# Performance work log

Measured on AMD Instinct MI355X. Metric: run time of the kernel, lower is better.

Reference implementation:

```python
import jax, jax.numpy as jnp
import numpy as np

INPUT_SIZE = 768
HIDDEN = [512, 256, 128]
LATENT = 32
NUM_LEVELS = 3
CODEBOOK_SIZE = 256
BATCH = 131072


def _init_linear(key, d_in, d_out):
    kw, kb = jax.random.split(key)
    lim = 1.0 / np.sqrt(d_in)
    W = jax.random.uniform(kw, (d_in, d_out), jnp.float32, -lim, lim)
    b = jax.random.uniform(kb, (d_out,), jnp.float32, -lim, lim)
    return W, b


def setup_inputs() -> dict:
    key = jax.random.key(0)
    keys = jax.random.split(key, 16)
    inp = {"x": jax.random.normal(keys[0], (BATCH, INPUT_SIZE), jnp.float32)}
    enc_dims = [INPUT_SIZE] + HIDDEN + [LATENT]          # 768->512->256->128->32
    dec_dims = [LATENT] + HIDDEN[::-1] + [INPUT_SIZE]     # 32->128->256->512->768
    for i in range(4):
        W, b = _init_linear(keys[1 + i], enc_dims[i], enc_dims[i + 1])
        inp[f"enc_W{i}"], inp[f"enc_b{i}"] = W, b
        W, b = _init_linear(keys[6 + i], dec_dims[i], dec_dims[i + 1])
        inp[f"dec_W{i}"], inp[f"dec_b{i}"] = W, b
    inp["codebooks"] = jax.random.normal(keys[12], (NUM_LEVELS, CODEBOOK_SIZE, LATENT), jnp.float32)
    return inp


def _mlp(x, Ws, bs):
    # Linear -> ReLU (-> Dropout p=0, identity) between layers, final layer linear.
    n = len(Ws)
    for i in range(n):
        x = x @ Ws[i] + bs[i]
        if i < n - 1:
            x = jax.nn.relu(x)
    return x


def _quantize(z, codebooks):
    # Residual vector quantization over NUM_LEVELS codebooks.
    L, K, D = codebooks.shape
    r = z
    idxs, rs, es = [], [], []
    for l in range(L):
        c = codebooks[l]                                  # [K, D]
        # squared-distance argmin (same argmin as cdist)
        d = jnp.sum(r * r, axis=-1, keepdims=True) - 2.0 * (r @ c.T) + jnp.sum(c * c, axis=-1)
        idx = jnp.argmin(d, axis=-1)                      # [B]
        e = c[idx]                                        # [B, D] gather
        idxs.append(idx)
        rs.append(r)
        es.append(e)
        r = r - e
    quantized = jnp.stack(idxs, axis=1)                   # [B, L] int codes
    r_stack = jnp.stack(rs, axis=1)                       # [B, L, D] residual inputs per level
    e_stack = jnp.stack(es, axis=1)                       # [B, L, D] selected embeddings
    sum_e = jnp.sum(e_stack, axis=1)                      # [B, D]
    # straight-through estimator
    z_hat = z + jax.lax.stop_gradient(sum_e - z)
    counts = jnp.sum(jax.nn.one_hot(quantized, K, dtype=jnp.float32), axis=0)  # [L, K] usage
    return quantized, r_stack, e_stack, z_hat, counts


def reference(x,
              enc_W0, enc_b0, enc_W1, enc_b1, enc_W2, enc_b2, enc_W3, enc_b3,
              dec_W0, dec_b0, dec_W1, dec_b1, dec_W2, dec_b2, dec_W3, dec_b3,
              codebooks):
    encoded = _mlp(x, [enc_W0, enc_W1, enc_W2, enc_W3], [enc_b0, enc_b1, enc_b2, enc_b3])
    quantized, r, e, z_hat, counts = _quantize(encoded, codebooks)
    decoded = _mlp(z_hat, [dec_W0, dec_W1, dec_W2, dec_W3], [dec_b0, dec_b1, dec_b2, dec_b3])
    return decoded, r, e, counts, quantized
```

## Files before the change

### kernel.cpp

```cpp
#include <hip/hip_runtime.h>
#include <hip/hip_bf16.h>
#include <cfloat>

#define B_TOTAL 131072
#define IN_DIM  768
#define NLEV    3
#define KCODE   256

typedef unsigned short u16;
typedef unsigned int   u32;
typedef __attribute__((ext_vector_type(8))) short bf16x8;
typedef __attribute__((ext_vector_type(4))) float f32x4;

#define GLOAD_LDS(g, l)                                                        \
    __builtin_amdgcn_global_load_lds(                                          \
        (const __attribute__((address_space(1))) u32*)(g),                     \
        (__attribute__((address_space(3))) u32*)(l), 16, 0, 0)

__device__ __forceinline__ u16 f2bf(float x) {
    union { __hip_bfloat16 h; u16 u; } c;
    c.h = __float2bfloat16(x);
    return c.u;
}
__device__ __forceinline__ float bf2f(u32 lo16) {
    union { u32 v; float f; } c;
    c.v = lo16 << 16;
    return c.f;
}
__device__ __forceinline__ u32 pack2(float a, float b) {
    return (u32)f2bf(a) | ((u32)f2bf(b) << 16);
}

template<int K, int N, bool AF32, bool RELU, bool OUTF32>
__global__ __launch_bounds__(256)
void gemm_mfma(const void* __restrict__ A_, const u16* __restrict__ Wt,
               const float* __restrict__ bias, void* __restrict__ C_)
{
    constexpr int NK  = K / 32;
    constexpr int NCB = N / 128;
    __shared__ u16 As[3][4096];
    __shared__ u16 Bs[3][4096];

    const int tid  = threadIdx.x;
    const int lane = tid & 63;
    const int wid  = tid >> 6;
    const int wrow = wid >> 1, wcol = wid & 1;

    const u32 nwg  = gridDim.x;
    const u32 orig = blockIdx.x;
    const u32 xcd = orig & 7u, q8 = nwg >> 3, r8 = nwg & 7u;
    const u32 wg = (xcd < r8 ? xcd * (q8 + 1) : r8 * (q8 + 1) + (xcd - r8) * q8)
                 + (orig >> 3);
    const int col0 = (int)(wg % NCB) * 128;
    const int row0 = (int)(wg / NCB) * 128;

    const u16*   Ab = (const u16*)A_;
    const float* Af = (const float*)A_;

    f32x4 acc[4][4];
    #pragma unroll
    for (int i = 0; i < 4; ++i)
        #pragma unroll
        for (int j = 0; j < 4; ++j) acc[i][j] = (f32x4){0.f, 0.f, 0.f, 0.f};

    auto stage_one = [&](u16* dstbase, const u16* src) {
        #pragma unroll
        for (int i = 0; i < 2; ++i) {
            const u32 o   = (u32)(i * 4096 + wid * 1024 + lane * 16);
            const u32 row = o >> 6;
            const u32 cbs = (o & 63u) ^ ((row & 3u) << 4);
            GLOAD_LDS((const char*)(src + (size_t)row * K) + cbs,
                      dstbase + (i * 2048 + wid * 512));
        }
    };
    auto stage_tile = [&](int buf, int kt) {
        stage_one(&Bs[buf][0], Wt + (size_t)col0 * K + kt * 32);
        stage_one(&As[buf][0], Ab + (size_t)row0 * K + kt * 32);
    };

    auto compute = [&](int buf) {
        const char* Ab8 = (const char*)&As[buf][0];
        const char* Bb8 = (const char*)&Bs[buf][0];
        const int kb = (lane >> 4) * 16;
        bf16x8 af[4], bf[4];
        #pragma unroll
        for (int mf = 0; mf < 4; ++mf) {
            const int r = wrow * 64 + mf * 16 + (lane & 15);
            af[mf] = *(const bf16x8*)(Ab8 + r * 64 + (kb ^ ((r & 3) << 4)));
        }
        #pragma unroll
        for (int nf = 0; nf < 4; ++nf) {
            const int r = wcol * 64 + nf * 16 + (lane & 15);
            bf[nf] = *(const bf16x8*)(Bb8 + r * 64 + (kb ^ ((r & 3) << 4)));
        }
        #pragma unroll
        for (int mf = 0; mf < 4; ++mf)
            #pragma unroll
            for (int nf = 0; nf < 4; ++nf)
                acc[mf][nf] = __builtin_amdgcn_mfma_f32_16x16x32_bf16(
                    af[mf], bf[nf], acc[mf][nf], 0, 0, 0);
    };

    if constexpr (AF32) {
        float4 fa[4];
        auto loadA = [&](int kt) {
            const int row = tid >> 1;
            const int ce0 = (tid & 1) * 16;
            const float* s = &Af[(size_t)(row0 + row) * K + kt * 32 + ce0];
            fa[0] = *(const float4*)(s + 0);
            fa[1] = *(const float4*)(s + 4);
            fa[2] = *(const float4*)(s + 8);
            fa[3] = *(const float4*)(s + 12);
        };
        auto writeA = [&](int buf) {
            const int row = tid >> 1;
            const int cb0 = (tid & 1) * 32;
            const int sw  = (row & 3) << 4;
            char* lb = (char*)&As[buf][0] + row * 64;
            *(uint4*)(lb + ((cb0 + 0) ^ sw)) = make_uint4(
                pack2(fa[0].x, fa[0].y), pack2(fa[0].z, fa[0].w),
                pack2(fa[1].x, fa[1].y), pack2(fa[1].z, fa[1].w));
            *(uint4*)(lb + ((cb0 + 16) ^ sw)) = make_uint4(
                pack2(fa[2].x, fa[2].y), pack2(fa[2].z, fa[2].w),
                pack2(fa[3].x, fa[3].y), pack2(fa[3].z, fa[3].w));
        };

        loadA(0);
        stage_one(&Bs[0][0], Wt + (size_t)col0 * K);
        writeA(0);
        if (NK > 1) {
            loadA(1);
            stage_one(&Bs[1][0], Wt + (size_t)col0 * K + 32);
        }

        #pragma unroll 1
        for (int kt = 0; kt < NK; ++kt) {
            if (kt == NK - 1) asm volatile("s_waitcnt vmcnt(0) lgkmcnt(0)");
            else              asm volatile("s_waitcnt vmcnt(6) lgkmcnt(0)");
            __builtin_amdgcn_sched_barrier(0);
            __builtin_amdgcn_s_barrier();
            __builtin_amdgcn_sched_barrier(0);
            if (kt + 1 < NK) writeA((kt + 1) % 3);
            if (kt + 2 < NK) {
                loadA(kt + 2);
                stage_one(&Bs[(kt + 2) % 3][0],
                          Wt + (size_t)col0 * K + (kt + 2) * 32);
            }
            compute(kt % 3);
        }
    } else {
        stage_tile(0, 0);
        if (NK > 1) stage_tile(1, 1);
        int cb_ = 0, sb_ = 2;
        #pragma unroll 1
        for (int kt = 0; kt < NK; ++kt) {
            if (kt == NK - 1) asm volatile("s_waitcnt vmcnt(0)");
            else              asm volatile("s_waitcnt vmcnt(4)");
            __builtin_amdgcn_sched_barrier(0);
            __builtin_amdgcn_s_barrier();
            __builtin_amdgcn_sched_barrier(0);
            if (kt + 2 < NK) stage_tile(sb_, kt + 2);
            compute(cb_);
            cb_ = (cb_ == 2) ? 0 : cb_ + 1;
            sb_ = (sb_ == 2) ? 0 : sb_ + 1;
        }
    }

    #pragma unroll
    for (int nf = 0; nf < 4; ++nf) {
        const int col = col0 + wcol * 64 + nf * 16 + (lane & 15);
        const float bv = bias[col];
        #pragma unroll
        for (int mf = 0; mf < 4; ++mf) {
            const int rbase = row0 + wrow * 64 + mf * 16 + (lane >> 4) * 4;
            #pragma unroll
            for (int r = 0; r < 4; ++r) {
                float o = acc[mf][nf][r] + bv;
                if (RELU) o = fmaxf(o, 0.f);
                if constexpr (OUTF32)
                    ((float*)C_)[(size_t)(rbase + r) * N + col] = o;
                else
                    ((u16*)C_)[(size_t)(rbase + r) * N + col] = f2bf(o);
            }
        }
    }
}

template<int K, int N>
__global__ __launch_bounds__(256)
void wcvt(const float* __restrict__ W, u16* __restrict__ Wt)
{
    const int idx = blockIdx.x * 256 + threadIdx.x;
    const int k = idx / N, n = idx - k * N;
    Wt[(size_t)n * K + k] = f2bf(W[idx]);
}

__global__ __launch_bounds__(256)
void vq_kernel(const u16* __restrict__ h3, const float* __restrict__ eW3,
               const float* __restrict__ eb3, const float* __restrict__ cb,
               float* __restrict__ r_out, float* __restrict__ e_out,
               float* __restrict__ q_out, u16* __restrict__ se_ws,
               u32* __restrict__ ghist, size_t grow_base)
{
    __shared__ float W3[128 * 32];
    __shared__ float ebv[32];
    __shared__ float clds[256 * 36];
    __shared__ float cc2[256];
    __shared__ u32   lh[NLEV * KCODE];

    const int tid = threadIdx.x;
    const size_t lrow = (size_t)blockIdx.x * 256 + tid;
    const size_t grow = grow_base + lrow;

    for (int i = tid; i < 128 * 32; i += 256) W3[i] = eW3[i];
    if (tid < 32) ebv[tid] = eb3[tid];
    for (int i = tid; i < NLEV * KCODE; i += 256) lh[i] = 0;
    __syncthreads();

    float r[32];
    #pragma unroll
    for (int j = 0; j < 32; ++j) r[j] = ebv[j];
    {
        const u32* hrow = (const u32*)h3 + lrow * 64;
        #pragma unroll 2
        for (int k2 = 0; k2 < 64; ++k2) {
            const u32 v = hrow[k2];
            const float x0 = bf2f(v & 0xffffu), x1 = bf2f(v >> 16);
            const float* w0 = &W3[(2 * k2) * 32];
            const float* w1 = &W3[(2 * k2 + 1) * 32];
            #pragma unroll
            for (int j4 = 0; j4 < 8; ++j4) {
                const float4 a = *(const float4*)&w0[4 * j4];
                const float4 b = *(const float4*)&w1[4 * j4];
                r[4*j4+0] = fmaf(x1, b.x, fmaf(x0, a.x, r[4*j4+0]));
                r[4*j4+1] = fmaf(x1, b.y, fmaf(x0, a.y, r[4*j4+1]));
                r[4*j4+2] = fmaf(x1, b.z, fmaf(x0, a.z, r[4*j4+2]));
                r[4*j4+3] = fmaf(x1, b.w, fmaf(x0, a.w, r[4*j4+3]));
            }
        }
    }

    float z0[32];
    #pragma unroll
    for (int j = 0; j < 32; ++j) z0[j] = r[j];

    #pragma unroll 1
    for (int l = 0; l < NLEV; ++l) {
        __syncthreads();
        {
            const float* cl = cb + ((size_t)l * KCODE + tid) * 32;
            float s = 0.f;
            #pragma unroll
            for (int m = 0; m < 8; ++m) {
                const float4 v = *(const float4*)&cl[4 * m];
                *(float4*)&clds[tid * 36 + 4 * m] = v;
                s = fmaf(v.x, v.x, s); s = fmaf(v.y, v.y, s);
                s = fmaf(v.z, v.z, s); s = fmaf(v.w, v.w, s);
            }
            cc2[tid] = -0.5f * s;
        }
        __syncthreads();

        float best = -FLT_MAX;
        int   bidx = 0;
        #pragma unroll 1
        for (int k = 0; k < KCODE; ++k) {
            const float* ck = &clds[k * 36];
            float d0 = 0.f, d1 = 0.f, d2 = 0.f, d3 = 0.f;
            #pragma unroll
            for (int m = 0; m < 8; m += 4) {
                const float4 v0 = *(const float4*)&ck[4 * (m + 0)];
                const float4 v1 = *(const float4*)&ck[4 * (m + 1)];
                const float4 v2 = *(const float4*)&ck[4 * (m + 2)];
                const float4 v3 = *(const float4*)&ck[4 * (m + 3)];
                d0 = fmaf(r[4*m+0],  v0.x, d0); d0 = fmaf(r[4*m+1],  v0.y, d0);
                d0 = fmaf(r[4*m+2],  v0.z, d0); d0 = fmaf(r[4*m+3],  v0.w, d0);
                d1 = fmaf(r[4*m+4],  v1.x, d1); d1 = fmaf(r[4*m+5],  v1.y, d1);
                d1 = fmaf(r[4*m+6],  v1.z, d1); d1 = fmaf(r[4*m+7],  v1.w, d1);
                d2 = fmaf(r[4*m+8],  v2.x, d2); d2 = fmaf(r[4*m+9],  v2.y, d2);
                d2 = fmaf(r[4*m+10], v2.z, d2); d2 = fmaf(r[4*m+11], v2.w, d2);
                d3 = fmaf(r[4*m+12], v3.x, d3); d3 = fmaf(r[4*m+13], v3.y, d3);
                d3 = fmaf(r[4*m+14], v3.z, d3); d3 = fmaf(r[4*m+15], v3.w, d3);
            }
            const float s = ((d0 + d1) + (d2 + d3)) + cc2[k];
            if (s > best) { best = s; bidx = k; }
        }

        const size_t base = (grow * NLEV + l) * 32;
        const float* ce = &clds[bidx * 36];
        #pragma unroll
        for (int m = 0; m < 8; ++m) {
            const float4 ev = *(const float4*)&ce[4 * m];
            *(float4*)&r_out[base + 4 * m] =
                make_float4(r[4*m+0], r[4*m+1], r[4*m+2], r[4*m+3]);
            *(float4*)&e_out[base + 4 * m] = ev;
            r[4*m+0] -= ev.x; r[4*m+1] -= ev.y;
            r[4*m+2] -= ev.z; r[4*m+3] -= ev.w;
        }
        q_out[grow * NLEV + l] = (float)bidx;
        atomicAdd(&lh[l * KCODE + bidx], 1u);
    }

    u32* sed = (u32*)se_ws + lrow * 16;
    #pragma unroll
    for (int m = 0; m < 16; ++m)
        sed[m] = pack2(z0[2*m] - r[2*m], z0[2*m+1] - r[2*m+1]);

    __syncthreads();
    for (int i = tid; i < NLEV * KCODE; i += 256)
        if (lh[i]) atomicAdd(&ghist[i], lh[i]);
}

__global__ void zero_hist(u32* h) {
    if (threadIdx.x < NLEV * KCODE) h[threadIdx.x] = 0;
}
__global__ void counts_fin(const u32* __restrict__ g, float* __restrict__ o) {
    if (threadIdx.x < NLEV * KCODE) o[threadIdx.x] = (float)g[threadIdx.x];
}

__global__ __launch_bounds__(256)
void counts_k(const float* __restrict__ q, float* __restrict__ cnt)
{
    const int l = blockIdx.x >> 8;
    const int k = blockIdx.x & 255;
    const float pat = (float)k;
    int c = 0;
    for (int i = threadIdx.x; i < B_TOTAL; i += 256)
        c += (q[(size_t)i * NLEV + l] == pat) ? 1 : 0;
    __shared__ int red[256];
    red[threadIdx.x] = c;
    __syncthreads();
    for (int s = 128; s > 0; s >>= 1) {
        if (threadIdx.x < s) red[threadIdx.x] += red[threadIdx.x + s];
        __syncthreads();
    }
    if (threadIdx.x == 0)
        cnt[blockIdx.x] = (float)red[0];
}

template<int K, int N, bool RELU, bool AGLOBAL>
static __device__ __forceinline__
void layer16(const float* __restrict__ A, size_t grow0,
             const float* __restrict__ W, const float* __restrict__ bias,
             float* __restrict__ C)
{
    constexpr int QPT = N / 128;
    const int tr = threadIdx.x >> 5;
    const int tc = threadIdx.x & 31;
    float acc[2][QPT * 4];
    #pragma unroll
    for (int i = 0; i < 2; ++i)
        #pragma unroll
        for (int j = 0; j < QPT * 4; ++j) acc[i][j] = 0.f;
    #pragma unroll 2
    for (int k0 = 0; k0 < K; k0 += 4) {
        float4 av[2];
        #pragma unroll
        for (int i = 0; i < 2; ++i) {
            if (AGLOBAL)
                av[i] = *(const float4*)&A[(grow0 + tr * 2 + i) * (size_t)K + k0];
            else
                av[i] = *(const float4*)&A[(tr * 2 + i) * K + k0];
        }
        #pragma unroll
        for (int kk = 0; kk < 4; ++kk) {
            #pragma unroll
            for (int q = 0; q < QPT; ++q) {
                const float4 w4 = *(const float4*)&W[(size_t)(k0 + kk) * N + 4 * (tc + 32 * q)];
                #pragma unroll
                for (int i = 0; i < 2; ++i) {
                    const float a = ((const float*)&av[i])[kk];
                    acc[i][4*q+0] = fmaf(a, w4.x, acc[i][4*q+0]);
                    acc[i][4*q+1] = fmaf(a, w4.y, acc[i][4*q+1]);
                    acc[i][4*q+2] = fmaf(a, w4.z, acc[i][4*q+2]);
                    acc[i][4*q+3] = fmaf(a, w4.w, acc[i][4*q+3]);
                }
            }
        }
    }
    #pragma unroll
    for (int q = 0; q < QPT; ++q) {
        const float4 b4 = *(const float4*)&bias[4 * (tc + 32 * q)];
        #pragma unroll
        for (int i = 0; i < 2; ++i) {
            float4 o;
            o.x = acc[i][4*q+0] + b4.x; o.y = acc[i][4*q+1] + b4.y;
            o.z = acc[i][4*q+2] + b4.z; o.w = acc[i][4*q+3] + b4.w;
            if (RELU) {
                o.x = fmaxf(o.x, 0.f); o.y = fmaxf(o.y, 0.f);
                o.z = fmaxf(o.z, 0.f); o.w = fmaxf(o.w, 0.f);
            }
            *(float4*)&C[(tr * 2 + i) * N + 4 * (tc + 32 * q)] = o;
        }
    }
}

static __device__ __forceinline__
void layer_final16(const float* __restrict__ A, const float* __restrict__ W,
                   const float* __restrict__ bias, float* __restrict__ Cg, size_t grow0)
{
    constexpr int QPT = 6;
    const int tr = threadIdx.x >> 5;
    const int tc = threadIdx.x & 31;
    float acc[2][QPT * 4];
    #pragma unroll
    for (int i = 0; i < 2; ++i)
        #pragma unroll
        for (int j = 0; j < QPT * 4; ++j) acc[i][j] = 0.f;
    #pragma unroll 2
    for (int k0 = 0; k0 < 512; k0 += 4) {
        float4 av[2];
        #pragma unroll
        for (int i = 0; i < 2; ++i)
            av[i] = *(const float4*)&A[(tr * 2 + i) * 512 + k0];
        #pragma unroll
        for (int kk = 0; kk < 4; ++kk) {
            #pragma unroll
            for (int q = 0; q < QPT; ++q) {
                const float4 w4 = *(const float4*)&W[(size_t)(k0 + kk) * 768 + 4 * (tc + 32 * q)];
                #pragma unroll
                for (int i = 0; i < 2; ++i) {
                    const float a = ((const float*)&av[i])[kk];
                    acc[i][4*q+0] = fmaf(a, w4.x, acc[i][4*q+0]);
                    acc[i][4*q+1] = fmaf(a, w4.y, acc[i][4*q+1]);
                    acc[i][4*q+2] = fmaf(a, w4.z, acc[i][4*q+2]);
                    acc[i][4*q+3] = fmaf(a, w4.w, acc[i][4*q+3]);
                }
            }
        }
    }
    #pragma unroll
    for (int q = 0; q < QPT; ++q) {
        const float4 b4 = *(const float4*)&bias[4 * (tc + 32 * q)];
        #pragma unroll
        for (int i = 0; i < 2; ++i) {
            float4 s;
            s.x = acc[i][4*q+0] + b4.x; s.y = acc[i][4*q+1] + b4.y;
            s.z = acc[i][4*q+2] + b4.z; s.w = acc[i][4*q+3] + b4.w;
            *(float4*)&Cg[(grow0 + tr * 2 + i) * (size_t)768 + 4 * (tc + 32 * q)] = s;
        }
    }
}

static __device__ __forceinline__
void layer_narrow16(const float* __restrict__ A, const float* __restrict__ W,
                    const float* __restrict__ bias, float* __restrict__ Z)
{
    const int row = threadIdx.x >> 4;
    const int g   = threadIdx.x & 15;
    float a0 = 0.f, a1 = 0.f;
    #pragma unroll 4
    for (int k0 = 0; k0 < 128; k0 += 4) {
        const float4 av = *(const float4*)&A[row * 128 + k0];
        #pragma unroll
        for (int kk = 0; kk < 4; ++kk) {
            const float2 w2 = *(const float2*)&W[(k0 + kk) * 32 + 2 * g];
            const float a = ((const float*)&av)[kk];
            a0 = fmaf(a, w2.x, a0);
            a1 = fmaf(a, w2.y, a1);
        }
    }
    Z[row * 36 + 2 * g + 0] = a0 + bias[2 * g + 0];
    Z[row * 36 + 2 * g + 1] = a1 + bias[2 * g + 1];
}

__global__ __launch_bounds__(256)
void enc_vq_kernel(const float* __restrict__ x,
                   const float* __restrict__ eW0, const float* __restrict__ eb0,
                   const float* __restrict__ eW1, const float* __restrict__ eb1,
                   const float* __restrict__ eW2, const float* __restrict__ eb2,
                   const float* __restrict__ eW3, const float* __restrict__ eb3,
                   const float* __restrict__ cb,
                   float* __restrict__ r_out, float* __restrict__ e_out,
                   float* __restrict__ q_out)
{
    __shared__ __align__(16) char smem[59648];
    float* h1   = (float*)(smem);
    float* h2   = (float*)(smem + 32768);
    float* h3   = (float*)(smem + 49152);
    float* z    = (float*)(smem + 57344);
    float* clds = (float*)(smem);
    float* cc   = (float*)(smem + 36864);

    const size_t grow0 = (size_t)blockIdx.x * 16;
    layer16<768, 512, true, true >(x,  grow0, eW0, eb0, h1);
    __syncthreads();
    layer16<512, 256, true, false>(h1, 0,     eW1, eb1, h2);
    __syncthreads();
    layer16<256, 128, true, false>(h2, 0,     eW2, eb2, h3);
    __syncthreads();
    layer_narrow16(h3, eW3, eb3, z);

    const int row = threadIdx.x >> 4;
    const int g   = threadIdx.x & 15;
    const size_t grow = grow0 + row;

    #pragma unroll 1
    for (int l = 0; l < NLEV; ++l) {
        __syncthreads();
        {
            const float* cl = cb + (size_t)l * KCODE * 32;
            const int t = threadIdx.x;
            float s = 0.f;
            #pragma unroll
            for (int m = 0; m < 8; ++m) {
                const float4 v = *(const float4*)&cl[t * 32 + 4 * m];
                *(float4*)&clds[t * 36 + 4 * m] = v;
                s = fmaf(v.x, v.x, s); s = fmaf(v.y, v.y, s);
                s = fmaf(v.z, v.z, s); s = fmaf(v.w, v.w, s);
            }
            cc[t] = s;
        }
        __syncthreads();

        float r[32];
        #pragma unroll
        for (int m = 0; m < 8; ++m) {
            const float4 v = *(const float4*)&z[row * 36 + 4 * m];
            r[4*m+0] = v.x; r[4*m+1] = v.y; r[4*m+2] = v.z; r[4*m+3] = v.w;
        }
        float rr = 0.f;
        #pragma unroll
        for (int j = 0; j < 32; ++j) rr = fmaf(r[j], r[j], rr);

        float best = FLT_MAX;
        int   bidx = 0x7fffffff;
        #pragma unroll 1
        for (int t = 0; t < 16; ++t) {
            const int k = g + 16 * t;
            const float* ck = &clds[k * 36];
            float d0 = 0.f, d1 = 0.f, d2 = 0.f, d3 = 0.f;
            #pragma unroll
            for (int m = 0; m < 8; m += 4) {
                const float4 v0 = *(const float4*)&ck[4 * (m + 0)];
                const float4 v1 = *(const float4*)&ck[4 * (m + 1)];
                const float4 v2 = *(const float4*)&ck[4 * (m + 2)];
                const float4 v3 = *(const float4*)&ck[4 * (m + 3)];
                d0 = fmaf(r[4*m+0],  v0.x, d0); d0 = fmaf(r[4*m+1],  v0.y, d0);
                d0 = fmaf(r[4*m+2],  v0.z, d0); d0 = fmaf(r[4*m+3],  v0.w, d0);
                d1 = fmaf(r[4*m+4],  v1.x, d1); d1 = fmaf(r[4*m+5],  v1.y, d1);
                d1 = fmaf(r[4*m+6],  v1.z, d1); d1 = fmaf(r[4*m+7],  v1.w, d1);
                d2 = fmaf(r[4*m+8],  v2.x, d2); d2 = fmaf(r[4*m+9],  v2.y, d2);
                d2 = fmaf(r[4*m+10], v2.z, d2); d2 = fmaf(r[4*m+11], v2.w, d2);
                d3 = fmaf(r[4*m+12], v3.x, d3); d3 = fmaf(r[4*m+13], v3.y, d3);
                d3 = fmaf(r[4*m+14], v3.z, d3); d3 = fmaf(r[4*m+15], v3.w, d3);
            }
            const float dot = (d0 + d1) + (d2 + d3);
            const float d = (rr - 2.f * dot) + cc[k];
            if (d < best || (d == best && k < bidx)) { best = d; bidx = k; }
        }
        #pragma unroll
        for (int off = 1; off < 16; off <<= 1) {
            const float ob = __shfl_xor(best, off);
            const int   oi = __shfl_xor(bidx, off);
            if (ob < best || (ob == best && oi < bidx)) { best = ob; bidx = oi; }
        }

        const float evx = clds[bidx * 36 + 2 * g + 0];
        const float evy = clds[bidx * 36 + 2 * g + 1];
        *(float2*)&r_out[(grow * NLEV + l) * 32 + 2 * g] = make_float2(r[2*g], r[2*g+1]);
        *(float2*)&e_out[(grow * NLEV + l) * 32 + 2 * g] = make_float2(evx, evy);
        if (g == 0) q_out[grow * NLEV + l] = (float)bidx;
        z[row * 36 + 2 * g + 0] = r[2 * g + 0] - evx;
        z[row * 36 + 2 * g + 1] = r[2 * g + 1] - evy;
    }
}

__global__ __launch_bounds__(256)
void dec_kernel(const float* __restrict__ e_in,
                const float* __restrict__ dW0, const float* __restrict__ db0,
                const float* __restrict__ dW1, const float* __restrict__ db1,
                const float* __restrict__ dW2, const float* __restrict__ db2,
                const float* __restrict__ dW3, const float* __restrict__ db3,
                float* __restrict__ dec_out)
{
    __shared__ __align__(16) char smem[59392];
    float* h3 = (float*)(smem);
    float* h2 = (float*)(smem + 32768);
    float* h1 = (float*)(smem + 49152);
    float* se = (float*)(smem + 57344);

    const size_t grow0 = (size_t)blockIdx.x * 16;
    const int row = threadIdx.x >> 4;
    const int g   = threadIdx.x & 15;
    {
        const size_t base = ((grow0 + row) * NLEV) * 32 + 2 * g;
        float s0 = 0.f, s1 = 0.f;
        #pragma unroll
        for (int l = 0; l < NLEV; ++l) {
            const float2 v = *(const float2*)&e_in[base + l * 32];
            s0 += v.x; s1 += v.y;
        }
        se[row * 32 + 2 * g + 0] = s0;
        se[row * 32 + 2 * g + 1] = s1;
    }
    __syncthreads();
    layer16<32,  128, true, false>(se, 0, dW0, db0, h1);
    __syncthreads();
    layer16<128, 256, true, false>(h1, 0, dW1, db1, h2);
    __syncthreads();
    layer16<256, 512, true, false>(h2, 0, dW2, db2, h3);
    __syncthreads();
    layer_final16(h3, dW3, db3, dec_out, grow0);
}

extern "C" void kernel_launch(void* const* d_in, const int* in_sizes, int n_in,
                              void* d_out, int out_size, void* d_ws, size_t ws_size,
                              hipStream_t stream)
{
    (void)in_sizes; (void)n_in; (void)out_size;
    const float* x  = (const float*)d_in[0];
    const float* cb = (const float*)d_in[17];
    const float *eW[4], *eb[4], *dW[4], *db[4];
    for (int i = 0; i < 4; ++i) {
        eW[i] = (const float*)d_in[1 + 4 * i];
        eb[i] = (const float*)d_in[2 + 4 * i];
        dW[i] = (const float*)d_in[3 + 4 * i];
        db[i] = (const float*)d_in[4 + 4 * i];
    }

    float* out = (float*)d_out;
    const size_t OFF_R = (size_t)B_TOTAL * IN_DIM;
    const size_t OFF_E = OFF_R + (size_t)B_TOTAL * NLEV * 32;
    const size_t OFF_C = OFF_E + (size_t)B_TOTAL * NLEV * 32;
    const size_t OFF_Q = OFF_C + (size_t)NLEV * KCODE;

    const size_t WTB = 2236416;
    size_t R = 0;
    for (size_t cand = 131072; cand >= 2048; cand >>= 1)
        if (WTB + cand * 3648 + 4096 <= ws_size) { R = cand; break; }

    if (R && d_ws) {
        u16* Wp   = (u16*)d_ws;
        u16* WtE0 = Wp;
        u16* WtE1 = WtE0 + 393216;
        u16* WtE2 = WtE1 + 131072;
        u16* WtD0 = WtE2 + 32768;
        u16* WtD1 = WtD0 + 4096;
        u16* WtD2 = WtD1 + 32768;
        u16* WtD3 = WtD2 + 131072;
        u16* h1   = WtD3 + 393216;
        u16* h2   = h1 + R * 512;
        u16* h3   = h2 + R * 256;
        u16* se   = h3 + R * 128;
        u16* d1   = se + R * 32;
        u16* d2   = d1 + R * 128;
        u16* d3   = d2 + R * 256;
        u32* ghist = (u32*)(d3 + R * 512);

        wcvt<768, 512><<<dim3((768 * 512) / 256), 256, 0, stream>>>(eW[0], WtE0);
        wcvt<512, 256><<<dim3((512 * 256) / 256), 256, 0, stream>>>(eW[1], WtE1);
        wcvt<256, 128><<<dim3((256 * 128) / 256), 256, 0, stream>>>(eW[2], WtE2);
        wcvt<32,  128><<<dim3((32 * 128) / 256),  256, 0, stream>>>(dW[0], WtD0);
        wcvt<128, 256><<<dim3((128 * 256) / 256), 256, 0, stream>>>(dW[1], WtD1);
        wcvt<256, 512><<<dim3((256 * 512) / 256), 256, 0, stream>>>(dW[2], WtD2);
        wcvt<512, 768><<<dim3((512 * 768) / 256), 256, 0, stream>>>(dW[3], WtD3);
        zero_hist<<<1, 768, 0, stream>>>(ghist);

        const int nch = B_TOTAL / (int)R;
        const int MB = (int)R / 128;
        for (int c = 0; c < nch; ++c) {
            const size_t rb = (size_t)c * R;
            gemm_mfma<768, 512, true,  true,  false><<<dim3(4 * MB), 256, 0, stream>>>(
                x + rb * 768, WtE0, eb[0], h1);
            gemm_mfma<512, 256, false, true,  false><<<dim3(2 * MB), 256, 0, stream>>>(
                h1, WtE1, eb[1], h2);
            gemm_mfma<256, 128, false, true,  false><<<dim3(1 * MB), 256, 0, stream>>>(
                h2, WtE2, eb[2], h3);
            vq_kernel<<<dim3((int)R / 256), 256, 0, stream>>>(
                h3, eW[3], eb[3], cb,
                out + OFF_R, out + OFF_E, out + OFF_Q, se, ghist, rb);
            gemm_mfma<32,  128, false, true,  false><<<dim3(1 * MB), 256, 0, stream>>>(
                se, WtD0, db[0], d1);
            gemm_mfma<128, 256, false, true,  false><<<dim3(2 * MB), 256, 0, stream>>>(
                d1, WtD1, db[1], d2);
            gemm_mfma<256, 512, false, true,  false><<<dim3(4 * MB), 256, 0, stream>>>(
                d2, WtD2, db[2], d3);
            gemm_mfma<512, 768, false, false, true ><<<dim3(6 * MB), 256, 0, stream>>>(
                d3, WtD3, db[3], out + rb * 768);
        }
        counts_fin<<<1, 768, 0, stream>>>(ghist, out + OFF_C);
    } else {
        enc_vq_kernel<<<dim3(B_TOTAL / 16), 256, 0, stream>>>(
            x, eW[0], eb[0], eW[1], eb[1], eW[2], eb[2], eW[3], eb[3], cb,
            out + OFF_R, out + OFF_E, out + OFF_Q);
        counts_k<<<dim3(NLEV * KCODE), 256, 0, stream>>>(out + OFF_Q, out + OFF_C);
        dec_kernel<<<dim3(B_TOTAL / 16), 256, 0, stream>>>(
            out + OFF_E, dW[0], db[0], dW[1], db[1], dW[2], db[2], dW[3], db[3], out);
    }
}
```

Baseline: 862.6 us.

## Enlarge GEMM block tile to 256x128 with 8 waves and MFMA priority

The MFMA GEMM block grows from 128x128 to 256x128 output rows by moving to 512 threads (8 waves), each wave still computing a 64x64 sub-tile. One staged weight (B) tile is now shared by twice as many rows, which halves B global/LDS staging per output and halves the number of workgroups launched. The A staging and vmcnt wait counts are adjusted to the new load counts, and s_setprio is raised around the MFMA loop to favour matrix issue. LDS per block rises to about 72KB and the grid shrinks, which may cut occupancy and leave CUs idle on the smaller layers.

```diff
diff --git a/kernel.cpp b/kernel.cpp
--- a/kernel.cpp
+++ b/kernel.cpp
@@ -32,19 +32,20 @@
 }
 
 template<int K, int N, bool AF32, bool RELU, bool OUTF32>
-__global__ __launch_bounds__(256)
+__global__ __launch_bounds__(512)
 void gemm_mfma(const void* __restrict__ A_, const u16* __restrict__ Wt,
                const float* __restrict__ bias, void* __restrict__ C_)
 {
     constexpr int NK  = K / 32;
     constexpr int NCB = N / 128;
-    __shared__ u16 As[3][4096];
+    __shared__ u16 As[3][8192];
     __shared__ u16 Bs[3][4096];
 
     const int tid  = threadIdx.x;
     const int lane = tid & 63;
     const int wid  = tid >> 6;
-    const int wrow = wid >> 1, wcol = wid & 1;
+    const int wrow = wid >> 1;
+    const int wcol = wid & 1;
 
     const u32 nwg  = gridDim.x;
     const u32 orig = blockIdx.x;
@@ -52,7 +53,7 @@
     const u32 wg = (xcd < r8 ? xcd * (q8 + 1) : r8 * (q8 + 1) + (xcd - r8) * q8)
                  + (orig >> 3);
     const int col0 = (int)(wg % NCB) * 128;
-    const int row0 = (int)(wg / NCB) * 128;
+    const int row0 = (int)(wg / NCB) * 256;
 
     const u16*   Ab = (const u16*)A_;
     const float* Af = (const float*)A_;
@@ -63,19 +64,26 @@
         #pragma unroll
         for (int j = 0; j < 4; ++j) acc[i][j] = (f32x4){0.f, 0.f, 0.f, 0.f};
 
-    auto stage_one = [&](u16* dstbase, const u16* src) {
+    auto stage_B = [&](u16* dstbase, const u16* src) {
+        const u32 o   = (u32)(tid * 16);
+        const u32 row = o >> 6;
+        const u32 cbs = (o & 63u) ^ ((row & 3u) << 4);
+        GLOAD_LDS((const char*)(src + (size_t)row * K) + cbs,
+                  dstbase + wid * 512);
+    };
+    auto stage_A = [&](u16* dstbase, const u16* src) {
         #pragma unroll
         for (int i = 0; i < 2; ++i) {
-            const u32 o   = (u32)(i * 4096 + wid * 1024 + lane * 16);
+            const u32 o   = (u32)(i * 8192 + tid * 16);
             const u32 row = o >> 6;
             const u32 cbs = (o & 63u) ^ ((row & 3u) << 4);
             GLOAD_LDS((const char*)(src + (size_t)row * K) + cbs,
-                      dstbase + (i * 2048 + wid * 512));
+                      dstbase + (i * 4096 + wid * 512));
         }
     };
     auto stage_tile = [&](int buf, int kt) {
-        stage_one(&Bs[buf][0], Wt + (size_t)col0 * K + kt * 32);
-        stage_one(&As[buf][0], Ab + (size_t)row0 * K + kt * 32);
+        stage_B(&Bs[buf][0], Wt + (size_t)col0 * K + kt * 32);
+        stage_A(&As[buf][0], Ab + (size_t)row0 * K + kt * 32);
     };
 
     auto compute = [&](int buf) {
@@ -93,12 +101,14 @@
             const int r = wcol * 64 + nf * 16 + (lane & 15);
             bf[nf] = *(const bf16x8*)(Bb8 + r * 64 + (kb ^ ((r & 3) << 4)));
         }
+        __builtin_amdgcn_s_setprio(1);
         #pragma unroll
         for (int mf = 0; mf < 4; ++mf)
             #pragma unroll
             for (int nf = 0; nf < 4; ++nf)
                 acc[mf][nf] = __builtin_amdgcn_mfma_f32_16x16x32_bf16(
                     af[mf], bf[nf], acc[mf][nf], 0, 0, 0);
+        __builtin_amdgcn_s_setprio(0);
     };
 
     if constexpr (AF32) {
@@ -126,25 +136,25 @@
         };
 
         loadA(0);
-        stage_one(&Bs[0][0], Wt + (size_t)col0 * K);
+        stage_B(&Bs[0][0], Wt + (size_t)col0 * K);
         writeA(0);
         if (NK > 1) {
             loadA(1);
-            stage_one(&Bs[1][0], Wt + (size_t)col0 * K + 32);
+            stage_B(&Bs[1][0], Wt + (size_t)col0 * K + 32);
         }
 
         #pragma unroll 1
         for (int kt = 0; kt < NK; ++kt) {
             if (kt == NK - 1) asm volatile("s_waitcnt vmcnt(0) lgkmcnt(0)");
-            else              asm volatile("s_waitcnt vmcnt(6) lgkmcnt(0)");
+            else              asm volatile("s_waitcnt vmcnt(5) lgkmcnt(0)");
             __builtin_amdgcn_sched_barrier(0);
             __builtin_amdgcn_s_barrier();
             __builtin_amdgcn_sched_barrier(0);
             if (kt + 1 < NK) writeA((kt + 1) % 3);
             if (kt + 2 < NK) {
                 loadA(kt + 2);
-                stage_one(&Bs[(kt + 2) % 3][0],
-                          Wt + (size_t)col0 * K + (kt + 2) * 32);
+                stage_B(&Bs[(kt + 2) % 3][0],
+                        Wt + (size_t)col0 * K + (kt + 2) * 32);
             }
             compute(kt % 3);
         }
@@ -155,7 +165,7 @@
         #pragma unroll 1
         for (int kt = 0; kt < NK; ++kt) {
             if (kt == NK - 1) asm volatile("s_waitcnt vmcnt(0)");
-            else              asm volatile("s_waitcnt vmcnt(4)");
+            else              asm volatile("s_waitcnt vmcnt(3)");
             __builtin_amdgcn_sched_barrier(0);
             __builtin_amdgcn_s_barrier();
             __builtin_amdgcn_sched_barrier(0);
@@ -658,25 +668,25 @@
         zero_hist<<<1, 768, 0, stream>>>(ghist);
 
         const int nch = B_TOTAL / (int)R;
-        const int MB = (int)R / 128;
+        const int MB2 = (int)R / 256;
         for (int c = 0; c < nch; ++c) {
             const size_t rb = (size_t)c * R;
-            gemm_mfma<768, 512, true,  true,  false><<<dim3(4 * MB), 256, 0, stream>>>(
+            gemm_mfma<768, 512, true,  true,  false><<<dim3(4 * MB2), 512, 0, stream>>>(
                 x + rb * 768, WtE0, eb[0], h1);
-            gemm_mfma<512, 256, false, true,  false><<<dim3(2 * MB), 256, 0, stream>>>(
+            gemm_mfma<512, 256, false, true,  false><<<dim3(2 * MB2), 512, 0, stream>>>(
                 h1, WtE1, eb[1], h2);
-            gemm_mfma<256, 128, false, true,  false><<<dim3(1 * MB), 256, 0, stream>>>(
+            gemm_mfma<256, 128, false, true,  false><<<dim3(1 * MB2), 512, 0, stream>>>(
                 h2, WtE2, eb[2], h3);
             vq_kernel<<<dim3((int)R / 256), 256, 0, stream>>>(
                 h3, eW[3], eb[3], cb,
                 out + OFF_R, out + OFF_E, out + OFF_Q, se, ghist, rb);
-            gemm_mfma<32,  128, false, true,  false><<<dim3(1 * MB), 256, 0, stream>>>(
+            gemm_mfma<32,  128, false, true,  false><<<dim3(1 * MB2), 512, 0, stream>>>(
                 se, WtD0, db[0], d1);
-            gemm_mfma<128, 256, false, true,  false><<<dim3(2 * MB), 256, 0, stream>>>(
+            gemm_mfma<128, 256, false, true,  false><<<dim3(2 * MB2), 512, 0, stream>>>(
                 d1, WtD1, db[1], d2);
-            gemm_mfma<256, 512, false, true,  false><<<dim3(4 * MB), 256, 0, stream>>>(
+            gemm_mfma<256, 512, false, true,  false><<<dim3(4 * MB2), 512, 0, stream>>>(
                 d2, WtD2, db[2], d3);
-            gemm_mfma<512, 768, false, false, true ><<<dim3(6 * MB), 256, 0, stream>>>(
+            gemm_mfma<512, 768, false, false, true ><<<dim3(6 * MB2), 512, 0, stream>>>(
                 d3, WtD3, db[3], out + rb * 768);
         }
         counts_fin<<<1, 768, 0, stream>>>(ghist, out + OFF_C);
```

Result: no change. 854.3 us (-1.0%).
